# Kernel tuning notes

Measured on AMD Instinct MI355X. Metric: run time of the kernel, lower is better.

The kernel has to match this reference:

```python
import jax, jax.numpy as jnp
import numpy as np

N2, T, E, D = 512, 4096, 512, 256  # G2 nodes, G1 type nodes, G1 entity nodes, embed dim


def setup_inputs() -> dict:
    key = jax.random.key(0)
    k = jax.random.split(key, 6)
    return {
        "all_node_embedding": jax.random.normal(k[0], (N2 + T, D), jnp.float32),
        "W2": jax.random.normal(k[1], (N2, N2, D), jnp.float32),
        "R2": jax.random.normal(k[2], (N2, N2, D), jnp.float32),
        "A1": jax.random.randint(k[3], (T, T), 0, 2, jnp.int32),
        "A2": jax.random.randint(k[4], (E, T), 0, 2, jnp.int32),
        "A3": jax.random.randint(k[5], (T, E), 0, 2, jnp.int32),
    }


def reference(all_node_embedding, W2, R2, A1, A2, A3):
    emb = all_node_embedding
    dt = emb.dtype
    n2, t = W2.shape[0], A1.shape[0]
    start = n2
    e = A2.shape[0]

    # --- G2_update: broadcast emb[i] over rows j, weight, add relation, sum over i ---
    x2 = emb[:n2]                                   # [N2, D]
    new2 = jnp.einsum("id,jid->jd", x2, W2) + R2.sum(1) + x2
    emb = emb.at[:n2].set(new2)

    # --- G1_sub1_update: every column filled -> full sum broadcast, degree-normalized gate ---
    sub = emb[start:start + t]                      # [T, D]
    S = sub.sum(0)                                  # [D], same for every row
    new1 = sub + S[None, :]
    deg1 = 1.0 + (A1 != 0).sum(1).astype(dt)        # [T] row nonzero counts + 1
    new1 = new1 * (1.0 - S[None, :] / deg1[:, None])
    emb = emb.at[start:start + t].set(new1)

    # --- G1_sub2: specific (entities) -> common (types); non-edges contribute ones ---
    A2f = (A2 != 0).astype(dt)                      # [E, T]
    spec = emb[:e]                                  # [E, D]
    deg2 = A2f.sum(0)                               # [T]
    msg2 = A2f.T @ spec + (e - deg2)[:, None]       # ones-filled background
    new_common = emb[start:start + t] + msg2
    emb = emb.at[start:start + t].set(new_common)

    # --- G1_sub3: common (types) -> specific (entities), degree-normalized gate ---
    A3f = (A3 != 0).astype(dt)                      # [T, E]
    deg3 = A3f.sum(0)                               # [E] column nonzero counts
    msg3 = A3f.T @ new_common + (t - deg3)[:, None]
    sum_arr = 1.0 + deg3                            # [E]
    new_spec = emb[:e] * (1.0 - msg3 / sum_arr[:, None])
    emb = emb.at[:e].set(new_spec)
    return emb
```

## Files before the change

### kernel.cpp

```cpp
#include <hip/hip_runtime.h>
#include <stdint.h>

#define DN 256
#define N2C 512
#define TC 4096
#define EC 512

#define B_K1 512
#define B_A  256

__global__ __launch_bounds__(512) void prep_fused(
    const float* __restrict__ emb, const float* __restrict__ W2,
    const float* __restrict__ R2, const int* __restrict__ A1,
    const int* __restrict__ A2, const int* __restrict__ A3,
    float* __restrict__ out, float* __restrict__ S,
    float* __restrict__ deg1, uint32_t* __restrict__ PT2,
    uint32_t* __restrict__ PT3)
{
    __shared__ __align__(16) char smem[64 * 65 * 4];
    uint32_t (*ldsb)[65] = (uint32_t (*)[65])smem;
    float4   (*red)[64]  = (float4 (*)[64])smem;

    const int bid = blockIdx.x;
    const int tid = threadIdx.x;

    if (bid < B_K1) {
        const int d4  = tid & 63;
        const int grp = tid >> 6;
        const int j   = bid;
        const float4* W = (const float4*)(W2 + (size_t)j * N2C * DN);
        const float4* R = (const float4*)(R2 + (size_t)j * N2C * DN);
        const float4* X = (const float4*)emb;

        float ax = 0.f, ay = 0.f, az = 0.f, aw = 0.f;
        const int i0 = grp * 64;
        #pragma unroll 4
        for (int i = i0; i < i0 + 64; ++i) {
            float4 w = W[i * 64 + d4];
            float4 r = R[i * 64 + d4];
            float4 x = X[i * 64 + d4];
            ax += x.x * w.x + r.x;
            ay += x.y * w.y + r.y;
            az += x.z * w.z + r.z;
            aw += x.w * w.w + r.w;
        }
        float4 mine; mine.x = ax; mine.y = ay; mine.z = az; mine.w = aw;
        red[grp][d4] = mine;
        __syncthreads();
        if (grp == 0) {
            float sx = 0.f, sy = 0.f, sz = 0.f, sw = 0.f;
            #pragma unroll
            for (int g = 0; g < 8; ++g) {
                float4 v = red[g][d4];
                sx += v.x; sy += v.y; sz += v.z; sw += v.w;
            }
            float4 x = X[j * 64 + d4];
            float4 o;
            o.x = sx + x.x; o.y = sy + x.y; o.z = sz + x.z; o.w = sw + x.w;
            ((float4*)out)[j * 64 + d4] = o;
        }
    } else {
        const int ab = bid - B_K1;

        {
            const int lane = tid & 63;
            #pragma unroll
            for (int it = 0; it < 2; ++it) {
                const int row = ab * 16 + it * 8 + (tid >> 6);
                const int4* p = (const int4*)(A1 + (size_t)row * TC);
                int cnt = 0;
                #pragma unroll
                for (int k = 0; k < 16; ++k) {
                    int4 v = p[k * 64 + lane];
                    cnt += (v.x != 0) + (v.y != 0) + (v.z != 0) + (v.w != 0);
                }
                #pragma unroll
                for (int off = 32; off > 0; off >>= 1)
                    cnt += __shfl_down(cnt, off, 64);
                if (lane == 0) deg1[row] = 1.0f + (float)cnt;
            }
        }

        #pragma unroll
        for (int pt = 0; pt < 2; ++pt) {
            const int sub = ab * 2 + pt;
            const int e0 = (sub & 7) * 64;
            const int t0 = (sub >> 3) * 64;
            const int tx = tid & 63;
            const int ty = tid >> 6;
            #pragma unroll
            for (int k = 0; k < 8; ++k) {
                int el = ty * 8 + k;
                ldsb[el][tx] = (A2[(size_t)(e0 + el) * TC + t0 + tx] != 0) ? 1u : 0u;
            }
            __syncthreads();
            if (tid < 128) {
                const int tl = tid & 63;
                const int w  = tid >> 6;
                uint32_t bits = 0;
                #pragma unroll
                for (int b = 0; b < 32; ++b) bits |= ldsb[w * 32 + b][tl] << b;
                PT2[(size_t)(t0 + tl) * 16 + (e0 >> 5) + w] = bits;
            }
            __syncthreads();
        }

        #pragma unroll
        for (int pt = 0; pt < 2; ++pt) {
            const int sub = ab * 2 + pt;
            const int t0 = (sub >> 3) * 64;
            const int e0 = (sub & 7) * 64;
            const int ex = tid & 63;
            const int ty = tid >> 6;
            #pragma unroll
            for (int k = 0; k < 8; ++k) {
                int tl = ty * 8 + k;
                ldsb[tl][ex] = (A3[(size_t)(t0 + tl) * EC + e0 + ex] != 0) ? 1u : 0u;
            }
            __syncthreads();
            if (tid < 128) {
                const int el = tid & 63;
                const int w  = tid >> 6;
                uint32_t bits = 0;
                #pragma unroll
                for (int b = 0; b < 32; ++b) bits |= ldsb[w * 32 + b][el] << b;
                PT3[(size_t)(e0 + el) * 128 + (t0 >> 5) + w] = bits;
            }
            __syncthreads();
        }

        {
            const int d = tid & 255;
            const int h = tid >> 8;
            const float* base = emb + (size_t)N2C * DN;
            const int r0 = ab * 16 + h * 8;
            float s = 0.f;
            #pragma unroll
            for (int r = r0; r < r0 + 8; ++r) s += base[(size_t)r * DN + d];
            atomicAdd(&S[d], s);
        }
    }
}

__global__ __launch_bounds__(256) void k3_dense(
    const float* __restrict__ emb, const uint32_t* __restrict__ PT2,
    const float* __restrict__ S, const float* __restrict__ deg1,
    float* out)
{
    const int d4 = threadIdx.x & 63;
    const int tg = threadIdx.x >> 6;
    const int t0 = blockIdx.x * 16 + tg * 4;
    const float4* spec = (const float4*)out;
    const uint32_t* pt = PT2 + (size_t)t0 * 16;

    float4 a0 = {0,0,0,0}, a1 = {0,0,0,0}, a2 = {0,0,0,0}, a3 = {0,0,0,0};
    int c0 = 0, c1 = 0, c2 = 0, c3 = 0;

    for (int ec = 0; ec < 16; ++ec) {
        const uint32_t w0 = pt[ec];
        const uint32_t w1 = pt[16 + ec];
        const uint32_t w2 = pt[32 + ec];
        const uint32_t w3 = pt[48 + ec];
        c0 += __popc(w0); c1 += __popc(w1); c2 += __popc(w2); c3 += __popc(w3);
        const float4* sp = spec + (size_t)ec * 32 * 64 + d4;
        #pragma unroll
        for (int b = 0; b < 32; ++b) {
            float4 v = sp[b * 64];
            float m0 = (float)((w0 >> b) & 1u);
            float m1 = (float)((w1 >> b) & 1u);
            float m2 = (float)((w2 >> b) & 1u);
            float m3 = (float)((w3 >> b) & 1u);
            a0.x = fmaf(m0, v.x, a0.x); a0.y = fmaf(m0, v.y, a0.y);
            a0.z = fmaf(m0, v.z, a0.z); a0.w = fmaf(m0, v.w, a0.w);
            a1.x = fmaf(m1, v.x, a1.x); a1.y = fmaf(m1, v.y, a1.y);
            a1.z = fmaf(m1, v.z, a1.z); a1.w = fmaf(m1, v.w, a1.w);
            a2.x = fmaf(m2, v.x, a2.x); a2.y = fmaf(m2, v.y, a2.y);
            a2.z = fmaf(m2, v.z, a2.z); a2.w = fmaf(m2, v.w, a2.w);
            a3.x = fmaf(m3, v.x, a3.x); a3.y = fmaf(m3, v.y, a3.y);
            a3.z = fmaf(m3, v.z, a3.z); a3.w = fmaf(m3, v.w, a3.w);
        }
    }

    const float4 Sv = ((const float4*)S)[d4];
#define K3_EPI(ak, ck, kk) { \
    const int t = t0 + kk; \
    const float inv = 1.0f / deg1[t]; \
    const float addc = (float)(EC - ck); \
    const float4 sub = ((const float4*)emb)[(size_t)(N2C + t) * 64 + d4]; \
    float4 o; \
    o.x = (sub.x + Sv.x) * (1.0f - Sv.x * inv) + ak.x + addc; \
    o.y = (sub.y + Sv.y) * (1.0f - Sv.y * inv) + ak.y + addc; \
    o.z = (sub.z + Sv.z) * (1.0f - Sv.z * inv) + ak.z + addc; \
    o.w = (sub.w + Sv.w) * (1.0f - Sv.w * inv) + ak.w + addc; \
    ((float4*)out)[(size_t)(N2C + t) * 64 + d4] = o; }
    K3_EPI(a0, c0, 0)
    K3_EPI(a1, c1, 1)
    K3_EPI(a2, c2, 2)
    K3_EPI(a3, c3, 3)
#undef K3_EPI
}

__global__ __launch_bounds__(256) void k4_part(
    const uint32_t* __restrict__ PT3, const float* __restrict__ out,
    float* __restrict__ P)
{
    const int d4    = threadIdx.x & 63;
    const int es    = threadIdx.x >> 6;
    const int etile = blockIdx.x >> 3;
    const int chunk = blockIdx.x & 7;
    const int e0 = etile * 16 + es * 4;
    const float4* nc = (const float4*)(out + (size_t)N2C * DN);

    float4 a0 = {0,0,0,0}, a1 = {0,0,0,0}, a2 = {0,0,0,0}, a3 = {0,0,0,0};

    for (int w = 0; w < 16; ++w) {
        const uint32_t m0 = PT3[(size_t)(e0 + 0) * 128 + chunk * 16 + w];
        const uint32_t m1 = PT3[(size_t)(e0 + 1) * 128 + chunk * 16 + w];
        const uint32_t m2 = PT3[(size_t)(e0 + 2) * 128 + chunk * 16 + w];
        const uint32_t m3 = PT3[(size_t)(e0 + 3) * 128 + chunk * 16 + w];
        const float4* np = nc + (size_t)((chunk * 16 + w) * 32) * 64 + d4;
        #pragma unroll
        for (int b = 0; b < 32; ++b) {
            float4 v = np[b * 64];
            float f0 = (float)((m0 >> b) & 1u);
            float f1 = (float)((m1 >> b) & 1u);
            float f2 = (float)((m2 >> b) & 1u);
            float f3 = (float)((m3 >> b) & 1u);
            a0.x = fmaf(f0, v.x, a0.x); a0.y = fmaf(f0, v.y, a0.y);
            a0.z = fmaf(f0, v.z, a0.z); a0.w = fmaf(f0, v.w, a0.w);
            a1.x = fmaf(f1, v.x, a1.x); a1.y = fmaf(f1, v.y, a1.y);
            a1.z = fmaf(f1, v.z, a1.z); a1.w = fmaf(f1, v.w, a1.w);
            a2.x = fmaf(f2, v.x, a2.x); a2.y = fmaf(f2, v.y, a2.y);
            a2.z = fmaf(f2, v.z, a2.z); a2.w = fmaf(f2, v.w, a2.w);
            a3.x = fmaf(f3, v.x, a3.x); a3.y = fmaf(f3, v.y, a3.y);
            a3.z = fmaf(f3, v.z, a3.z); a3.w = fmaf(f3, v.w, a3.w);
        }
    }
    float4* Pp = (float4*)P;
    Pp[((size_t)chunk * EC + e0 + 0) * 64 + d4] = a0;
    Pp[((size_t)chunk * EC + e0 + 1) * 64 + d4] = a1;
    Pp[((size_t)chunk * EC + e0 + 2) * 64 + d4] = a2;
    Pp[((size_t)chunk * EC + e0 + 3) * 64 + d4] = a3;
}

__global__ __launch_bounds__(256) void k4_fin(
    const uint32_t* __restrict__ PT3, const float* __restrict__ P,
    float* out)
{
    const int d4 = threadIdx.x & 63;
    const int es = threadIdx.x >> 6;
    const int e  = blockIdx.x * 4 + es;
    const float4* Pp = (const float4*)P;

    float4 s = {0.f, 0.f, 0.f, 0.f};
    #pragma unroll
    for (int c = 0; c < 8; ++c) {
        float4 v = Pp[((size_t)c * EC + e) * 64 + d4];
        s.x += v.x; s.y += v.y; s.z += v.z; s.w += v.w;
    }

    int c = __popc(PT3[(size_t)e * 128 + 2 * d4]) +
            __popc(PT3[(size_t)e * 128 + 2 * d4 + 1]);
    #pragma unroll
    for (int off = 32; off > 0; off >>= 1) c += __shfl_xor(c, off, 64);

    const float msg_add = (float)(TC - c);
    const float inv = 1.0f / (1.0f + (float)c);
    float4 cur = ((const float4*)out)[(size_t)e * 64 + d4];
    float4 o;
    o.x = cur.x * (1.0f - (s.x + msg_add) * inv);
    o.y = cur.y * (1.0f - (s.y + msg_add) * inv);
    o.z = cur.z * (1.0f - (s.z + msg_add) * inv);
    o.w = cur.w * (1.0f - (s.w + msg_add) * inv);
    ((float4*)out)[(size_t)e * 64 + d4] = o;
}

extern "C" void kernel_launch(void* const* d_in, const int* in_sizes, int n_in,
                              void* d_out, int out_size, void* d_ws, size_t ws_size,
                              hipStream_t stream) {
    const float* emb = (const float*)d_in[0];
    const float* W2  = (const float*)d_in[1];
    const float* R2  = (const float*)d_in[2];
    const int*   A1  = (const int*)d_in[3];
    const int*   A2  = (const int*)d_in[4];
    const int*   A3  = (const int*)d_in[5];
    float* out = (float*)d_out;

    float*    S    = (float*)d_ws;
    float*    deg1 = S + DN;
    uint32_t* PT2  = (uint32_t*)(deg1 + TC);
    uint32_t* PT3  = PT2 + (size_t)TC * 16;
    float*    P    = (float*)(PT3 + (size_t)EC * 128);

    hipMemsetAsync(d_ws, 0, DN * sizeof(float), stream);

    prep_fused<<<B_K1 + B_A, 512, 0, stream>>>(emb, W2, R2, A1, A2, A3,
                                               out, S, deg1, PT2, PT3);
    k3_dense<<<TC / 16, 256, 0, stream>>>(emb, PT2, S, deg1, out);
    k4_part<<<256, 256, 0, stream>>>(PT3, out, P);
    k4_fin<<<EC / 4, 256, 0, stream>>>(PT3, P, out);
}
```

Before: 215.9 us.

## Split G2 reduction over more blocks and shrink per-block work across kernels

Each G2 row reduction is now split into four quarter blocks of 256 threads that write partial sums to workspace, and a new combine kernel adds the partials plus the residual. Prep blocks shrink to 256 threads with a higher occupancy bound. The dense k3 and k4 kernels now handle two rows per wave instead of four, doubling their grid sizes. The goal is more parallelism and occupancy for the bandwidth-bound W2/R2 streaming. The costs are an extra kernel launch, a workspace round trip, and less reuse of each loaded vector in k3/k4.

```diff
diff --git a/kernel.cpp b/kernel.cpp
--- a/kernel.cpp
+++ b/kernel.cpp
@@ -6,16 +6,16 @@
 #define TC 4096
 #define EC 512
 
-#define B_K1 512
-#define B_A  256
-
-__global__ __launch_bounds__(512) void prep_fused(
+#define B_A   256
+#define B_TOT (B_A + 2048)
+
+__global__ __launch_bounds__(256, 8) void prep_fused(
     const float* __restrict__ emb, const float* __restrict__ W2,
     const float* __restrict__ R2, const int* __restrict__ A1,
     const int* __restrict__ A2, const int* __restrict__ A3,
-    float* __restrict__ out, float* __restrict__ S,
-    float* __restrict__ deg1, uint32_t* __restrict__ PT2,
-    uint32_t* __restrict__ PT3)
+    float* __restrict__ S, float* __restrict__ deg1,
+    uint32_t* __restrict__ PT2, uint32_t* __restrict__ PT3,
+    float* __restrict__ Ppart)
 {
     __shared__ __align__(16) char smem[64 * 65 * 4];
     uint32_t (*ldsb)[65] = (uint32_t (*)[65])smem;
@@ -24,18 +24,20 @@
     const int bid = blockIdx.x;
     const int tid = threadIdx.x;
 
-    if (bid < B_K1) {
+    if (bid >= B_A) {
+        const int kb  = bid - B_A;
+        const int j   = kb >> 2;
+        const int q   = kb & 3;
         const int d4  = tid & 63;
         const int grp = tid >> 6;
-        const int j   = bid;
         const float4* W = (const float4*)(W2 + (size_t)j * N2C * DN);
         const float4* R = (const float4*)(R2 + (size_t)j * N2C * DN);
         const float4* X = (const float4*)emb;
 
         float ax = 0.f, ay = 0.f, az = 0.f, aw = 0.f;
-        const int i0 = grp * 64;
+        const int i0 = q * 128 + grp * 32;
         #pragma unroll 4
-        for (int i = i0; i < i0 + 64; ++i) {
+        for (int i = i0; i < i0 + 32; ++i) {
             float4 w = W[i * 64 + d4];
             float4 r = R[i * 64 + d4];
             float4 x = X[i * 64 + d4];
@@ -48,28 +50,25 @@
         red[grp][d4] = mine;
         __syncthreads();
         if (grp == 0) {
-            float sx = 0.f, sy = 0.f, sz = 0.f, sw = 0.f;
-            #pragma unroll
-            for (int g = 0; g < 8; ++g) {
-                float4 v = red[g][d4];
-                sx += v.x; sy += v.y; sz += v.z; sw += v.w;
-            }
-            float4 x = X[j * 64 + d4];
+            float4 v0 = red[0][d4], v1 = red[1][d4];
+            float4 v2 = red[2][d4], v3 = red[3][d4];
             float4 o;
-            o.x = sx + x.x; o.y = sy + x.y; o.z = sz + x.z; o.w = sw + x.w;
-            ((float4*)out)[j * 64 + d4] = o;
+            o.x = (v0.x + v1.x) + (v2.x + v3.x);
+            o.y = (v0.y + v1.y) + (v2.y + v3.y);
+            o.z = (v0.z + v1.z) + (v2.z + v3.z);
+            o.w = (v0.w + v1.w) + (v2.w + v3.w);
+            ((float4*)Ppart)[(size_t)kb * 64 + d4] = o;
         }
     } else {
-        const int ab = bid - B_K1;
+        const int ab = bid;
 
         {
             const int lane = tid & 63;
-            #pragma unroll
-            for (int it = 0; it < 2; ++it) {
-                const int row = ab * 16 + it * 8 + (tid >> 6);
+            for (int it = 0; it < 4; ++it) {
+                const int row = ab * 16 + it * 4 + (tid >> 6);
                 const int4* p = (const int4*)(A1 + (size_t)row * TC);
                 int cnt = 0;
-                #pragma unroll
+                #pragma unroll 4
                 for (int k = 0; k < 16; ++k) {
                     int4 v = p[k * 64 + lane];
                     cnt += (v.x != 0) + (v.y != 0) + (v.z != 0) + (v.w != 0);
@@ -81,16 +80,16 @@
             }
         }
 
-        #pragma unroll
         for (int pt = 0; pt < 2; ++pt) {
             const int sub = ab * 2 + pt;
             const int e0 = (sub & 7) * 64;
             const int t0 = (sub >> 3) * 64;
             const int tx = tid & 63;
             const int ty = tid >> 6;
-            #pragma unroll
-            for (int k = 0; k < 8; ++k) {
-                int el = ty * 8 + k;
+            __syncthreads();
+            #pragma unroll 4
+            for (int k = 0; k < 16; ++k) {
+                int el = ty * 16 + k;
                 ldsb[el][tx] = (A2[(size_t)(e0 + el) * TC + t0 + tx] != 0) ? 1u : 0u;
             }
             __syncthreads();
@@ -102,19 +101,18 @@
                 for (int b = 0; b < 32; ++b) bits |= ldsb[w * 32 + b][tl] << b;
                 PT2[(size_t)(t0 + tl) * 16 + (e0 >> 5) + w] = bits;
             }
-            __syncthreads();
-        }
-
-        #pragma unroll
+        }
+
         for (int pt = 0; pt < 2; ++pt) {
             const int sub = ab * 2 + pt;
             const int t0 = (sub >> 3) * 64;
             const int e0 = (sub & 7) * 64;
             const int ex = tid & 63;
             const int ty = tid >> 6;
-            #pragma unroll
-            for (int k = 0; k < 8; ++k) {
-                int tl = ty * 8 + k;
+            __syncthreads();
+            #pragma unroll 4
+            for (int k = 0; k < 16; ++k) {
+                int tl = ty * 16 + k;
                 ldsb[tl][ex] = (A3[(size_t)(t0 + tl) * EC + e0 + ex] != 0) ? 1u : 0u;
             }
             __syncthreads();
@@ -126,20 +124,38 @@
                 for (int b = 0; b < 32; ++b) bits |= ldsb[w * 32 + b][el] << b;
                 PT3[(size_t)(e0 + el) * 128 + (t0 >> 5) + w] = bits;
             }
-            __syncthreads();
         }
 
         {
-            const int d = tid & 255;
-            const int h = tid >> 8;
+            const int d = tid;
             const float* base = emb + (size_t)N2C * DN;
-            const int r0 = ab * 16 + h * 8;
+            const int r0 = ab * 16;
             float s = 0.f;
-            #pragma unroll
-            for (int r = r0; r < r0 + 8; ++r) s += base[(size_t)r * DN + d];
+            #pragma unroll 4
+            for (int r = r0; r < r0 + 16; ++r) s += base[(size_t)r * DN + d];
             atomicAdd(&S[d], s);
         }
     }
+}
+
+__global__ __launch_bounds__(256) void k1_combine(
+    const float* __restrict__ emb, const float* __restrict__ Ppart,
+    float* __restrict__ out)
+{
+    const int jj = blockIdx.x * 4 + (threadIdx.x >> 6);
+    const int d4 = threadIdx.x & 63;
+    const float4* Pp = (const float4*)Ppart;
+    float4 v0 = Pp[(size_t)(jj * 4 + 0) * 64 + d4];
+    float4 v1 = Pp[(size_t)(jj * 4 + 1) * 64 + d4];
+    float4 v2 = Pp[(size_t)(jj * 4 + 2) * 64 + d4];
+    float4 v3 = Pp[(size_t)(jj * 4 + 3) * 64 + d4];
+    float4 x  = ((const float4*)emb)[(size_t)jj * 64 + d4];
+    float4 o;
+    o.x = (v0.x + v1.x) + (v2.x + v3.x) + x.x;
+    o.y = (v0.y + v1.y) + (v2.y + v3.y) + x.y;
+    o.z = (v0.z + v1.z) + (v2.z + v3.z) + x.z;
+    o.w = (v0.w + v1.w) + (v2.w + v3.w) + x.w;
+    ((float4*)out)[(size_t)jj * 64 + d4] = o;
 }
 
 __global__ __launch_bounds__(256) void k3_dense(
@@ -149,35 +165,27 @@
 {
     const int d4 = threadIdx.x & 63;
     const int tg = threadIdx.x >> 6;
-    const int t0 = blockIdx.x * 16 + tg * 4;
+    const int t0 = blockIdx.x * 8 + tg * 2;
     const float4* spec = (const float4*)out;
     const uint32_t* pt = PT2 + (size_t)t0 * 16;
 
-    float4 a0 = {0,0,0,0}, a1 = {0,0,0,0}, a2 = {0,0,0,0}, a3 = {0,0,0,0};
-    int c0 = 0, c1 = 0, c2 = 0, c3 = 0;
+    float4 a0 = {0,0,0,0}, a1 = {0,0,0,0};
+    int c0 = 0, c1 = 0;
 
     for (int ec = 0; ec < 16; ++ec) {
         const uint32_t w0 = pt[ec];
         const uint32_t w1 = pt[16 + ec];
-        const uint32_t w2 = pt[32 + ec];
-        const uint32_t w3 = pt[48 + ec];
-        c0 += __popc(w0); c1 += __popc(w1); c2 += __popc(w2); c3 += __popc(w3);
+        c0 += __popc(w0); c1 += __popc(w1);
         const float4* sp = spec + (size_t)ec * 32 * 64 + d4;
         #pragma unroll
         for (int b = 0; b < 32; ++b) {
             float4 v = sp[b * 64];
             float m0 = (float)((w0 >> b) & 1u);
             float m1 = (float)((w1 >> b) & 1u);
-            float m2 = (float)((w2 >> b) & 1u);
-            float m3 = (float)((w3 >> b) & 1u);
             a0.x = fmaf(m0, v.x, a0.x); a0.y = fmaf(m0, v.y, a0.y);
             a0.z = fmaf(m0, v.z, a0.z); a0.w = fmaf(m0, v.w, a0.w);
             a1.x = fmaf(m1, v.x, a1.x); a1.y = fmaf(m1, v.y, a1.y);
             a1.z = fmaf(m1, v.z, a1.z); a1.w = fmaf(m1, v.w, a1.w);
-            a2.x = fmaf(m2, v.x, a2.x); a2.y = fmaf(m2, v.y, a2.y);
-            a2.z = fmaf(m2, v.z, a2.z); a2.w = fmaf(m2, v.w, a2.w);
-            a3.x = fmaf(m3, v.x, a3.x); a3.y = fmaf(m3, v.y, a3.y);
-            a3.z = fmaf(m3, v.z, a3.z); a3.w = fmaf(m3, v.w, a3.w);
         }
     }
 
@@ -195,8 +203,6 @@
     ((float4*)out)[(size_t)(N2C + t) * 64 + d4] = o; }
     K3_EPI(a0, c0, 0)
     K3_EPI(a1, c1, 1)
-    K3_EPI(a2, c2, 2)
-    K3_EPI(a3, c3, 3)
 #undef K3_EPI
 }
 
@@ -208,39 +214,29 @@
     const int es    = threadIdx.x >> 6;
     const int etile = blockIdx.x >> 3;
     const int chunk = blockIdx.x & 7;
-    const int e0 = etile * 16 + es * 4;
+    const int e0 = etile * 8 + es * 2;
     const float4* nc = (const float4*)(out + (size_t)N2C * DN);
 
-    float4 a0 = {0,0,0,0}, a1 = {0,0,0,0}, a2 = {0,0,0,0}, a3 = {0,0,0,0};
+    float4 a0 = {0,0,0,0}, a1 = {0,0,0,0};
 
     for (int w = 0; w < 16; ++w) {
         const uint32_t m0 = PT3[(size_t)(e0 + 0) * 128 + chunk * 16 + w];
         const uint32_t m1 = PT3[(size_t)(e0 + 1) * 128 + chunk * 16 + w];
-        const uint32_t m2 = PT3[(size_t)(e0 + 2) * 128 + chunk * 16 + w];
-        const uint32_t m3 = PT3[(size_t)(e0 + 3) * 128 + chunk * 16 + w];
         const float4* np = nc + (size_t)((chunk * 16 + w) * 32) * 64 + d4;
         #pragma unroll
         for (int b = 0; b < 32; ++b) {
             float4 v = np[b * 64];
             float f0 = (float)((m0 >> b) & 1u);
             float f1 = (float)((m1 >> b) & 1u);
-            float f2 = (float)((m2 >> b) & 1u);
-            float f3 = (float)((m3 >> b) & 1u);
             a0.x = fmaf(f0, v.x, a0.x); a0.y = fmaf(f0, v.y, a0.y);
             a0.z = fmaf(f0, v.z, a0.z); a0.w = fmaf(f0, v.w, a0.w);
             a1.x = fmaf(f1, v.x, a1.x); a1.y = fmaf(f1, v.y, a1.y);
             a1.z = fmaf(f1, v.z, a1.z); a1.w = fmaf(f1, v.w, a1.w);
-            a2.x = fmaf(f2, v.x, a2.x); a2.y = fmaf(f2, v.y, a2.y);
-            a2.z = fmaf(f2, v.z, a2.z); a2.w = fmaf(f2, v.w, a2.w);
-            a3.x = fmaf(f3, v.x, a3.x); a3.y = fmaf(f3, v.y, a3.y);
-            a3.z = fmaf(f3, v.z, a3.z); a3.w = fmaf(f3, v.w, a3.w);
         }
     }
     float4* Pp = (float4*)P;
     Pp[((size_t)chunk * EC + e0 + 0) * 64 + d4] = a0;
     Pp[((size_t)chunk * EC + e0 + 1) * 64 + d4] = a1;
-    Pp[((size_t)chunk * EC + e0 + 2) * 64 + d4] = a2;
-    Pp[((size_t)chunk * EC + e0 + 3) * 64 + d4] = a3;
 }
 
 __global__ __launch_bounds__(256) void k4_fin(
@@ -291,12 +287,14 @@
     uint32_t* PT2  = (uint32_t*)(deg1 + TC);
     uint32_t* PT3  = PT2 + (size_t)TC * 16;
     float*    P    = (float*)(PT3 + (size_t)EC * 128);
+    float*    Ppart = P;
 
     hipMemsetAsync(d_ws, 0, DN * sizeof(float), stream);
 
-    prep_fused<<<B_K1 + B_A, 512, 0, stream>>>(emb, W2, R2, A1, A2, A3,
-                                               out, S, deg1, PT2, PT3);
-    k3_dense<<<TC / 16, 256, 0, stream>>>(emb, PT2, S, deg1, out);
-    k4_part<<<256, 256, 0, stream>>>(PT3, out, P);
+    prep_fused<<<B_TOT, 256, 0, stream>>>(emb, W2, R2, A1, A2, A3,
+                                          S, deg1, PT2, PT3, Ppart);
+    k1_combine<<<N2C / 4, 256, 0, stream>>>(emb, Ppart, out);
+    k3_dense<<<TC / 8, 256, 0, stream>>>(emb, PT2, S, deg1, out);
+    k4_part<<<512, 256, 0, stream>>>(PT3, out, P);
     k4_fin<<<EC / 4, 256, 0, stream>>>(PT3, P, out);
 }
```

New measurement: 212.4 us. No clear change (-1.6%).
